# Optimization experiments

Hardware: AMD Instinct MI355X
Metric: run time of the kernel (lower is better)

Reference implementation:

```python
import jax, jax.numpy as jnp
import numpy as np

B, T, SEQ = 8, 129, 128
H, N, NL, NE, V = 512, 64, 4, 128, 18

def _gelu(x):
    return jax.nn.gelu(x, approximate=False)

def _conv2d(x, w, b, stride):
    y = jax.lax.conv_general_dilated(x, w, (stride, stride), 'VALID',
                                     dimension_numbers=('NCHW', 'OIHW', 'NCHW'))
    return y + b[None, :, None, None]

def _layernorm(x, g, b, eps=1e-5):
    mu = jnp.mean(x, axis=-1, keepdims=True)
    var = jnp.mean(jnp.square(x - mu), axis=-1, keepdims=True)
    return (x - mu) * jax.lax.rsqrt(var + eps) * g + b

def _s4_kernel(log_dt, A_re, A_im, C_re, C_im, L):
    # Diagonal SSM (ZOH discretization, B=1): K[h,l] = 2*Re(sum_n Ceff * exp(dt*A)^l)
    dt = jnp.exp(log_dt)[:, None]                  # [H,1]
    A = A_re + 1j * A_im                            # [H,N] complex64
    dtA = (dt * A).astype(jnp.complex64)
    C = (C_re + 1j * C_im).astype(jnp.complex64)
    Ceff = C * (jnp.exp(dtA) - 1.0) / A             # [H,N]
    vand = jnp.exp(dtA[:, :, None] * jnp.arange(L, dtype=jnp.float32))  # [H,N,L]
    return 2.0 * jnp.einsum('hn,hnl->hl', Ceff, vand).real

def _fft_conv(u, K, D):
    # u: [B,H,L]  K: [H,L]  causal conv via zero-padded FFT
    L = u.shape[-1]
    n = 2 * L
    Uf = jnp.fft.rfft(u, n=n)
    Kf = jnp.fft.rfft(K, n=n)
    y = jnp.fft.irfft(Uf * Kf[None], n=n)[..., :L]
    return y + D[None, :, None] * u

def setup_inputs() -> dict:
    key = jax.random.key(0)
    ks = jax.random.split(key, 32)
    d = {}
    d['states'] = jax.random.uniform(ks[0], (B, T, 4, 84, 84), dtype=jnp.float32)
    d['actions'] = jax.random.randint(ks[1], (B, T), 0, V)
    d['rtgs'] = jax.random.uniform(ks[2], (B, T, 1), dtype=jnp.float32)
    s = 0.02
    d['enc_w1'] = jax.random.normal(ks[3], (32, 4, 8, 8)) * s
    d['enc_b1'] = jnp.zeros((32,))
    d['enc_w2'] = jax.random.normal(ks[4], (64, 32, 4, 4)) * s
    d['enc_b2'] = jnp.zeros((64,))
    d['enc_w3'] = jax.random.normal(ks[5], (64, 64, 3, 3)) * s
    d['enc_b3'] = jnp.zeros((64,))
    d['enc_lw'] = jax.random.normal(ks[6], (3136, NE)) * s
    d['enc_lb'] = jnp.zeros((NE,))
    d['ret_w'] = jax.random.normal(ks[7], (1, NE)) * s
    d['ret_b'] = jnp.zeros((NE,))
    d['act_emb'] = jax.random.normal(ks[8], (V, NE)) * s
    d['proj_w'] = jax.random.normal(ks[9], (3 * NE, H)) * s
    d['proj_b'] = jnp.zeros((H,))
    d['pre_w'] = jax.random.normal(ks[10], (H, H)) * s
    d['pre_b'] = jnp.zeros((H,))
    d['ln_g'] = jnp.ones((NL, H))
    d['ln_b'] = jnp.zeros((NL, H))
    lo, hi = np.log(1e-3), np.log(1e-1)
    d['log_dt'] = lo + jax.random.uniform(ks[11], (NL, H)) * (hi - lo)
    d['A_re'] = -0.5 * jnp.ones((NL, H, N))
    d['A_im'] = jnp.broadcast_to(np.pi * jnp.arange(N, dtype=jnp.float32), (NL, H, N)).copy()
    d['C_re'] = jax.random.normal(ks[12], (NL, H, N)) * (0.5 ** 0.5)
    d['C_im'] = jax.random.normal(ks[13], (NL, H, N)) * (0.5 ** 0.5)
    d['Dp'] = jax.random.normal(ks[14], (NL, H))
    d['aft_w'] = jax.random.normal(ks[15], (NL, H, H)) * s
    d['aft_b'] = jnp.zeros((NL, H))
    d['out_w'] = jax.random.normal(ks[16], (H, V)) * s
    return d

def reference(states, actions, rtgs, enc_w1, enc_b1, enc_w2, enc_b2, enc_w3, enc_b3,
              enc_lw, enc_lb, ret_w, ret_b, act_emb, proj_w, proj_b, pre_w, pre_b,
              ln_g, ln_b, log_dt, A_re, A_im, C_re, C_im, Dp, aft_w, aft_b, out_w):
    S = actions.shape[1] - 1  # del_r = 1
    # state encoder over B*S frames
    x = states[:, 1:].reshape(-1, 4, 84, 84)
    x = jax.nn.relu(_conv2d(x, enc_w1, enc_b1, 4))
    x = jax.nn.relu(_conv2d(x, enc_w2, enc_b2, 2))
    x = jax.nn.relu(_conv2d(x, enc_w3, enc_b3, 1))
    se = jnp.tanh(x.reshape(x.shape[0], -1) @ enc_lw + enc_lb)          # [B*S, NE]
    ae = jnp.tanh(act_emb[actions[:, :S].reshape(-1)])                   # [B*S, NE]
    re = jnp.tanh(rtgs[:, :S].reshape(-1, 1) @ ret_w + ret_b)            # [B*S, NE]
    u = jnp.concatenate([se, ae, re], axis=-1) @ proj_w + proj_b
    u = u.reshape(states.shape[0], S, H)
    y = _gelu(u) @ pre_w + pre_b                                          # beforeblock
    for i in range(NL):
        r = _layernorm(y, ln_g[i], ln_b[i])
        v = jnp.transpose(r, (0, 2, 1))                                   # [B,H,S]
        K = _s4_kernel(log_dt[i], A_re[i], A_im[i], C_re[i], C_im[i], S)
        c = _fft_conv(v, K, Dp[i])
        c = jnp.transpose(c, (0, 2, 1))                                   # [B,S,H]
        c = _gelu(_gelu(c) @ aft_w[i] + aft_b[i])
        y = c + y                                                          # s4_resnet
    logits = y @ out_w                                                     # [B,S,V]
    return logits
```

## Files before the change

### kernel.cpp

```cpp
#include <hip/hip_runtime.h>

#define Bq 8
#define Tq 129
#define Sq 128
#define Hq 512
#define Nq 64
#define NLq 4
#define NEq 128
#define Vq 18

typedef unsigned short u16;
typedef unsigned int u32;
typedef __attribute__((ext_vector_type(8))) short short8v;
typedef __attribute__((ext_vector_type(4))) float f32x4;

__device__ __forceinline__ float gelu_f(float x) {
  return 0.5f * x * (1.0f + erff(x * 0.70710678118654752f));
}

__device__ __forceinline__ u16 f2b(float x) {
  union { float f; unsigned int u; } v; v.f = x;
  unsigned int r = v.u + 0x7FFFu + ((v.u >> 16) & 1u);
  return (u16)(r >> 16);
}

__device__ __forceinline__ float b2f_lo(u32 u) {
  union { unsigned int u; float f; } v; v.u = u << 16; return v.f;
}
__device__ __forceinline__ float b2f_hi(u32 u) {
  union { unsigned int u; float f; } v; v.u = u & 0xffff0000u; return v.f;
}

__global__ __launch_bounds__(256) void prep_k(
    const float* __restrict__ enc_lw, const float* __restrict__ proj_w,
    const float* __restrict__ pre_w, const float* __restrict__ aft_w,
    const float* __restrict__ out_w,
    const float* __restrict__ w1, const float* __restrict__ w2,
    const float* __restrict__ w3,
    u16* __restrict__ Wt_enc, u16* __restrict__ Wt_proj, u16* __restrict__ Wt_pre,
    u16* __restrict__ Wt_aft, u16* __restrict__ Wt_out,
    u16* __restrict__ B1t, u16* __restrict__ B2t, u16* __restrict__ B3t) {
  __shared__ u16 T[64][65];
  int bid = blockIdx.x;
  if (bid >= 474) {
    int i = (bid - 474) * 256 + threadIdx.x;
    if (i < 8192) {
      int n = i >> 8, k = i & 255;
      int ic = k >> 6, ky = (k >> 3) & 7, kx = k & 7;
      B1t[i] = f2b(w1[((n * 4 + ic) * 8 + ky) * 8 + kx]);
    } else if (i < 8192 + 32768) {
      int j = i - 8192;
      int n = j >> 9, k = j & 511;
      int kyx = k >> 5, ic = k & 31, ky = kyx >> 2, kx = kyx & 3;
      B2t[j] = f2b(w2[((n * 32 + ic) * 4 + ky) * 4 + kx]);
    } else if (i < 8192 + 32768 + 36864) {
      int j = i - 40960;
      int n = j / 576, k = j - n * 576;
      int ic = k & 63, kyx = k >> 6, ky = kyx / 3, kx = kyx % 3;
      B3t[j] = f2b(w3[((n * 64 + ic) * 3 + ky) * 3 + kx]);
    }
    return;
  }
  const float* src; u16* dst; int K, N, kt, nt, t;
  if (bid < 98)       { t = bid;       src = enc_lw; dst = Wt_enc;  K = 3136; N = 128; kt = t >> 1; nt = t & 1; }
  else if (bid < 146) { t = bid - 98;  src = proj_w; dst = Wt_proj; K = 384;  N = 512; kt = t >> 3; nt = t & 7; }
  else if (bid < 210) { t = bid - 146; src = pre_w;  dst = Wt_pre;  K = 512;  N = 512; kt = t >> 3; nt = t & 7; }
  else if (bid < 466) { t = bid - 210; int L = t >> 6; t &= 63;
                        src = aft_w + (size_t)L * 262144; dst = Wt_aft + (size_t)L * 262144;
                        K = 512; N = 512; kt = t >> 3; nt = t & 7; }
  else                { t = bid - 466; src = out_w;  dst = Wt_out;  K = 512;  N = 18;  kt = t;      nt = 0; }
  int k0 = kt * 64, n0 = nt * 64;
  #pragma unroll
  for (int it = 0; it < 16; it++) {
    int idx = it * 256 + threadIdx.x;
    int rr = idx >> 6, cc = idx & 63;
    float v = (n0 + cc < N) ? src[(size_t)(k0 + rr) * N + n0 + cc] : 0.f;
    T[cc][rr] = f2b(v);
  }
  __syncthreads();
  #pragma unroll
  for (int it = 0; it < 16; it++) {
    int idx = it * 256 + threadIdx.x;
    int rr = idx >> 6, cc = idx & 63;
    dst[(size_t)(n0 + rr) * K + k0 + cc] = T[rr][cc];
  }
}

template<bool AF32, int EPI>
__global__ __launch_bounds__(256) void mgemm(const void* __restrict__ Av,
    const u16* __restrict__ Wt, const float* __restrict__ bias,
    const float* __restrict__ res, void* __restrict__ Cv,
    int M, int K, int N, int ldc) {
  __shared__ u16 As[4][64][40];
  __shared__ u16 Bs[4][64][40];
  int tid = threadIdx.x;
  int bn = blockIdx.x * 64, bm = blockIdx.y * 64;
  int lane = tid & 63, w = tid >> 6;
  int q = lane >> 4, r = lane & 15;
  int wm = (w >> 1) * 32, wn = (w & 1) * 32;
  int am = tid >> 2, ak0 = (tid & 3) * 8;
  f32x4 acc[2][2] = {};
  for (int k0 = 0; k0 < K; k0 += 128) {
    #pragma unroll
    for (int st = 0; st < 4; st++) {
      int kk = k0 + st * 32 + ak0;
      if constexpr (AF32) {
        const float* A = (const float*)Av;
        const float* src = A + (size_t)(bm + am) * K + kk;
        float4 v0 = *(const float4*)src;
        float4 v1 = *(const float4*)(src + 4);
        ushort4 lo, hi;
        lo.x = f2b(v0.x); lo.y = f2b(v0.y); lo.z = f2b(v0.z); lo.w = f2b(v0.w);
        hi.x = f2b(v1.x); hi.y = f2b(v1.y); hi.z = f2b(v1.z); hi.w = f2b(v1.w);
        *(ushort4*)&As[st][am][ak0] = lo;
        *(ushort4*)&As[st][am][ak0 + 4] = hi;
      } else {
        *(short8v*)&As[st][am][ak0] =
            *(const short8v*)((const u16*)Av + (size_t)(bm + am) * K + kk);
      }
      *(short8v*)&Bs[st][am][ak0] = *(const short8v*)(Wt + (size_t)(bn + am) * K + kk);
    }
    __syncthreads();
    #pragma unroll
    for (int st = 0; st < 4; st++) {
      short8v a0 = *(const short8v*)&As[st][wm + r][q * 8];
      short8v a1 = *(const short8v*)&As[st][wm + 16 + r][q * 8];
      short8v b0 = *(const short8v*)&Bs[st][wn + r][q * 8];
      short8v b1 = *(const short8v*)&Bs[st][wn + 16 + r][q * 8];
      acc[0][0] = __builtin_amdgcn_mfma_f32_16x16x32_bf16(a0, b0, acc[0][0], 0, 0, 0);
      acc[0][1] = __builtin_amdgcn_mfma_f32_16x16x32_bf16(a0, b1, acc[0][1], 0, 0, 0);
      acc[1][0] = __builtin_amdgcn_mfma_f32_16x16x32_bf16(a1, b0, acc[1][0], 0, 0, 0);
      acc[1][1] = __builtin_amdgcn_mfma_f32_16x16x32_bf16(a1, b1, acc[1][1], 0, 0, 0);
    }
    __syncthreads();
  }
  #pragma unroll
  for (int ms = 0; ms < 2; ms++) {
    #pragma unroll
    for (int ns = 0; ns < 2; ns++) {
      #pragma unroll
      for (int reg = 0; reg < 4; reg++) {
        int m = bm + wm + ms * 16 + q * 4 + reg;
        int n = bn + wn + ns * 16 + r;
        if (n < N) {
          float v = acc[ms][ns][reg] + (bias ? bias[n] : 0.f);
          if (EPI == 0) ((float*)Cv)[(size_t)m * ldc + n] = v;
          if (EPI == 2) ((u16*)Cv)[(size_t)m * ldc + n] = f2b(gelu_f(v));
          if (EPI == 3) ((float*)Cv)[(size_t)m * ldc + n] = gelu_f(v) + res[(size_t)m * ldc + n];
        }
      }
    }
  }
}

__global__ __launch_bounds__(256) void enc_gemm(const u16* __restrict__ A,
    const u16* __restrict__ Wt, float* __restrict__ Cp) {
  __shared__ u16 As[64][40];
  __shared__ u16 Bs[64][40];
  int tid = threadIdx.x;
  int bn = blockIdx.x * 64, bm = blockIdx.y * 64, kc = blockIdx.z;
  int lane = tid & 63, w = tid >> 6;
  int q = lane >> 4, r = lane & 15;
  int wm = (w >> 1) * 32, wn = (w & 1) * 32;
  int am = tid >> 2, ak = (tid & 3) * 8;
  f32x4 acc[2][2] = {};
  int kend = kc * 448 + 448;
  for (int k0 = kc * 448; k0 < kend; k0 += 32) {
    *(short8v*)&As[am][ak] = *(const short8v*)(A + (size_t)(bm + am) * 3136 + k0 + ak);
    *(short8v*)&Bs[am][ak] = *(const short8v*)(Wt + (size_t)(bn + am) * 3136 + k0 + ak);
    __syncthreads();
    short8v a0 = *(const short8v*)&As[wm + r][q * 8];
    short8v a1 = *(const short8v*)&As[wm + 16 + r][q * 8];
    short8v b0 = *(const short8v*)&Bs[wn + r][q * 8];
    short8v b1 = *(const short8v*)&Bs[wn + 16 + r][q * 8];
    acc[0][0] = __builtin_amdgcn_mfma_f32_16x16x32_bf16(a0, b0, acc[0][0], 0, 0, 0);
    acc[0][1] = __builtin_amdgcn_mfma_f32_16x16x32_bf16(a0, b1, acc[0][1], 0, 0, 0);
    acc[1][0] = __builtin_amdgcn_mfma_f32_16x16x32_bf16(a1, b0, acc[1][0], 0, 0, 0);
    acc[1][1] = __builtin_amdgcn_mfma_f32_16x16x32_bf16(a1, b1, acc[1][1], 0, 0, 0);
    __syncthreads();
  }
  #pragma unroll
  for (int ms = 0; ms < 2; ms++)
    #pragma unroll
    for (int ns = 0; ns < 2; ns++)
      #pragma unroll
      for (int reg = 0; reg < 4; reg++) {
        int m = bm + wm + ms * 16 + q * 4 + reg;
        int n = bn + wn + ns * 16 + r;
        Cp[(size_t)(kc * 1024 + m) * 128 + n] = acc[ms][ns][reg];
      }
}

__global__ __launch_bounds__(256) void embedred_k(const float* __restrict__ Cp,
    const float* __restrict__ enc_lb, const int* __restrict__ actions,
    const float* __restrict__ rtgs, const float* __restrict__ act_emb,
    const float* __restrict__ ret_w, const float* __restrict__ ret_b,
    u16* __restrict__ uin) {
  int f = blockIdx.x;
  int b = f >> 7, s = f & 127;
  int e = threadIdx.x;
  if (e < 128) {
    float sum = enc_lb[e];
    #pragma unroll
    for (int kc = 0; kc < 7; kc++) sum += Cp[(size_t)(kc * 1024 + f) * 128 + e];
    uin[(size_t)f * 384 + e] = f2b(tanhf(sum));
    uin[(size_t)f * 384 + 256 + e] =
        f2b(tanhf(fmaf(rtgs[b * Tq + s], ret_w[e], ret_b[e])));
  } else {
    int ee = e - 128;
    int a = actions[b * Tq + s];
    uin[(size_t)f * 384 + 128 + ee] = f2b(tanhf(act_emb[a * NEq + ee]));
  }
}

__global__ __launch_bounds__(512) void conv1_mfma(const float* __restrict__ states,
    const u16* __restrict__ B1t, const float* __restrict__ bias, u16* __restrict__ out) {
  __shared__ u16 lds[28224];
  int fr = blockIdx.x;
  int b = fr >> 7, s = fr & 127;
  const float* in = states + (size_t)(b * Tq + s + 1) * 28224;
  int tid = threadIdx.x;
  #pragma unroll
  for (int it = 0; it < 14; it++) {
    int idx = tid + it * 512;
    if (idx < 7056) {
      float4 v = ((const float4*)in)[idx];
      ushort4 uv;
      uv.x = f2b(v.x); uv.y = f2b(v.y); uv.z = f2b(v.z); uv.w = f2b(v.w);
      *(ushort4*)&lds[idx * 4] = uv;
    }
  }
  int lane = tid & 63, w = tid >> 6;
  int q = lane >> 4, r = lane & 15;
  short8v bfr[2][8];
  #pragma unroll
  for (int nt = 0; nt < 2; nt++)
    #pragma unroll
    for (int ks = 0; ks < 8; ks++)
      bfr[nt][ks] = *(const short8v*)(B1t + (nt * 16 + r) * 256 + ks * 32 + q * 8);
  __syncthreads();
  for (int mt = w; mt < 25; mt += 8) {
    int m = mt * 16 + r;
    int oy = m / 20, ox = m % 20;
    f32x4 acc0 = {0.f, 0.f, 0.f, 0.f}, acc1 = {0.f, 0.f, 0.f, 0.f};
    #pragma unroll
    for (int ks = 0; ks < 8; ks++) {
      int k0 = ks * 32 + q * 8;
      int ic = k0 >> 6, ky = (k0 >> 3) & 7;
      int ai = ic * 7056 + (oy * 4 + ky) * 84 + ox * 4;
      ushort4 lo = *(const ushort4*)&lds[ai];
      ushort4 hi = *(const ushort4*)&lds[ai + 4];
      short8v av;
      av[0] = (short)lo.x; av[1] = (short)lo.y; av[2] = (short)lo.z; av[3] = (short)lo.w;
      av[4] = (short)hi.x; av[5] = (short)hi.y; av[6] = (short)hi.z; av[7] = (short)hi.w;
      acc0 = __builtin_amdgcn_mfma_f32_16x16x32_bf16(av, bfr[0][ks], acc0, 0, 0, 0);
      acc1 = __builtin_amdgcn_mfma_f32_16x16x32_bf16(av, bfr[1][ks], acc1, 0, 0, 0);
    }
    #pragma unroll
    for (int reg = 0; reg < 4; reg++) {
      int pos = mt * 16 + q * 4 + reg;
      out[(size_t)fr * 12800 + pos * 32 + r]      = f2b(fmaxf(acc0[reg] + bias[r], 0.f));
      out[(size_t)fr * 12800 + pos * 32 + 16 + r] = f2b(fmaxf(acc1[reg] + bias[16 + r], 0.f));
    }
  }
}

__global__ __launch_bounds__(256) void conv2_mfma(const u16* __restrict__ in_,
    const u16* __restrict__ B2t, const float* __restrict__ bias, u16* __restrict__ out) {
  __shared__ u16 lds[12800];
  int fr = blockIdx.x;
  int tid = threadIdx.x;
  const short8v* src = (const short8v*)(in_ + (size_t)fr * 12800);
  short8v* dst = (short8v*)lds;
  #pragma unroll
  for (int it = 0; it < 7; it++) {
    int idx = tid + it * 256;
    if (idx < 1600) dst[idx] = src[idx];
  }
  int lane = tid & 63, w = tid >> 6;
  int q = lane >> 4, r = lane & 15;
  int n = w * 16 + r;
  short8v bfr[16];
  #pragma unroll
  for (int ks = 0; ks < 16; ks++)
    bfr[ks] = *(const short8v*)(B2t + n * 512 + ks * 32 + q * 8);
  __syncthreads();
  float bn = bias[n];
  #pragma unroll
  for (int mt = 0; mt < 6; mt++) {
    int m = mt * 16 + r; if (m > 80) m = 80;
    int oy = m / 9, ox = m % 9;
    f32x4 acc = {0.f, 0.f, 0.f, 0.f};
    #pragma unroll
    for (int ks = 0; ks < 16; ks++) {
      int ky = ks >> 2, kx = ks & 3;
      int ai = ((oy * 2 + ky) * 20 + ox * 2 + kx) * 32 + q * 8;
      short8v av = *(const short8v*)&lds[ai];
      acc = __builtin_amdgcn_mfma_f32_16x16x32_bf16(av, bfr[ks], acc, 0, 0, 0);
    }
    #pragma unroll
    for (int reg = 0; reg < 4; reg++) {
      int pos = mt * 16 + q * 4 + reg;
      if (pos < 81)
        out[(size_t)fr * 5184 + pos * 64 + n] = f2b(fmaxf(acc[reg] + bn, 0.f));
    }
  }
}

__global__ __launch_bounds__(256) void conv3_mfma(const u16* __restrict__ in_,
    const u16* __restrict__ B3t, const float* __restrict__ bias, u16* __restrict__ out) {
  __shared__ u16 lds[5184];
  int fr = blockIdx.x;
  int tid = threadIdx.x;
  const short8v* src = (const short8v*)(in_ + (size_t)fr * 5184);
  short8v* dst = (short8v*)lds;
  #pragma unroll
  for (int it = 0; it < 3; it++) {
    int idx = tid + it * 256;
    if (idx < 648) dst[idx] = src[idx];
  }
  int lane = tid & 63, w = tid >> 6;
  int q = lane >> 4, r = lane & 15;
  int n = w * 16 + r;
  short8v bfr[18];
  #pragma unroll
  for (int ks = 0; ks < 18; ks++)
    bfr[ks] = *(const short8v*)(B3t + n * 576 + ks * 32 + q * 8);
  __syncthreads();
  float bn = bias[n];
  #pragma unroll
  for (int mt = 0; mt < 4; mt++) {
    int m = mt * 16 + r; if (m > 48) m = 48;
    int oy = m / 7, ox = m % 7;
    f32x4 acc = {0.f, 0.f, 0.f, 0.f};
    #pragma unroll
    for (int ks = 0; ks < 18; ks++) {
      int kyx = ks >> 1;
      int ky = kyx / 3, kx = kyx % 3;
      int ic0 = (ks & 1) * 32 + q * 8;
      int ai = ((oy + ky) * 9 + ox + kx) * 64 + ic0;
      short8v av = *(const short8v*)&lds[ai];
      acc = __builtin_amdgcn_mfma_f32_16x16x32_bf16(av, bfr[ks], acc, 0, 0, 0);
    }
    #pragma unroll
    for (int reg = 0; reg < 4; reg++) {
      int pos = mt * 16 + q * 4 + reg;
      if (pos < 49)
        out[(size_t)fr * 3136 + n * 49 + pos] = f2b(fmaxf(acc[reg] + bn, 0.f));
    }
  }
}

__global__ __launch_bounds__(64) void s4k_gen(const float* __restrict__ log_dt,
    const float* __restrict__ A_re, const float* __restrict__ A_im,
    const float* __restrict__ C_re, const float* __restrict__ C_im,
    u16* __restrict__ Ktb) {
  __shared__ float con[64][129];
  int lh = blockIdx.x;
  int n = threadIdx.x;
  float dt = expf(log_dt[lh]);
  float ar = A_re[(size_t)lh * Nq + n], ai = A_im[(size_t)lh * Nq + n];
  float al = dt * ar, be = dt * ai;
  float er = expf(al);
  float wr = er * cosf(be), wi = er * sinf(be);
  float zr = wr - 1.0f, zi = wi;
  float den = 1.0f / (ar * ar + ai * ai);
  float tr = (zr * ar + zi * ai) * den, ti = (zi * ar - zr * ai) * den;
  float Cr = C_re[(size_t)lh * Nq + n], Ci = C_im[(size_t)lh * Nq + n];
  float cr = Cr * tr - Ci * ti, ci = Cr * ti + Ci * tr;
  float curr = 1.0f, curi = 0.0f;
  for (int l = 0; l < Sq; l++) {
    con[n][l] = cr * curr - ci * curi;
    float nr = curr * wr - curi * wi;
    curi = curr * wi + curi * wr;
    curr = nr;
  }
  __syncthreads();
  int layer = lh >> 9, h = lh & 511;
  #pragma unroll
  for (int li = n; li < Sq; li += 64) {
    float s = 0.f;
    for (int j = 0; j < 64; j++) s += con[j][li];
    Ktb[((size_t)layer * Sq + li) * Hq + h] = f2b(2.0f * s);
  }
}

__global__ __launch_bounds__(256) void ln_stats(const float* __restrict__ y,
    float2* __restrict__ stats) {
  int row = blockIdx.x * 4 + (threadIdx.x >> 6);
  int lane = threadIdx.x & 63;
  const float* x = y + (size_t)row * Hq;
  float s = 0.f, s2 = 0.f;
  #pragma unroll
  for (int j = 0; j < 8; j++) {
    float v = x[lane + j * 64];
    s += v; s2 += v * v;
  }
  #pragma unroll
  for (int o = 32; o >= 1; o >>= 1) {
    s += __shfl_xor(s, o);
    s2 += __shfl_xor(s2, o);
  }
  if (lane == 0) {
    float mu = s * (1.f / Hq);
    float var = s2 * (1.f / Hq) - mu * mu;
    stats[row] = make_float2(mu, rsqrtf(var + 1e-5f));
  }
}

__global__ __launch_bounds__(256) void sconv_fused(const float* __restrict__ y,
    const float2* __restrict__ stats, const float* __restrict__ g,
    const float* __restrict__ bta, const u16* __restrict__ Kt,
    const float* __restrict__ D, u16* __restrict__ cact) {
  __shared__ u32 P[16][140];
  __shared__ u32 KL[16][132];
  int hc = blockIdx.x, b = blockIdx.y;
  int t = threadIdx.x;
  int h0 = hc * 32;
  if (t < 16) {
    #pragma unroll
    for (int i = 0; i < 8; i++) P[t][i] = 0;
  }
  #pragma unroll
  for (int it = 0; it < 8; it++) {
    int idx = it * 256 + t;
    int p = idx & 15, j = idx >> 4;
    KL[p][j] = *(const u32*)(Kt + (size_t)j * Hq + h0 + 2 * p);
  }
  #pragma unroll
  for (int it = 0; it < 8; it++) {
    int idx = it * 256 + t;
    int p = idx & 15, s = idx >> 4;
    int row = b * Sq + s;
    float2 v = *(const float2*)(y + (size_t)row * Hq + h0 + 2 * p);
    float2 st = stats[row];
    float2 gg = *(const float2*)(g + h0 + 2 * p);
    float2 bb = *(const float2*)(bta + h0 + 2 * p);
    float r0 = (v.x - st.x) * st.y * gg.x + bb.x;
    float r1 = (v.y - st.x) * st.y * gg.y + bb.y;
    P[p][8 + s] = (u32)f2b(r0) | ((u32)f2b(r1) << 16);
  }
  __syncthreads();
  int p = t & 15, sg = t >> 4;
  int s0 = sg * 8;
  float acc0[8], acc1[8];
  float2 d2 = *(const float2*)(D + h0 + 2 * p);
  #pragma unroll
  for (int k = 0; k < 8; k++) {
    u32 rv = P[p][8 + s0 + k];
    acc0[k] = d2.x * b2f_lo(rv);
    acc1[k] = d2.y * b2f_hi(rv);
  }
  for (int jb = 0; jb <= sg; jb++) {
    int base = (sg - jb) * 8;
    u32 wv[16], kv[8];
    *(uint4*)&wv[0]  = *(const uint4*)&P[p][base];
    *(uint4*)&wv[4]  = *(const uint4*)&P[p][base + 4];
    *(uint4*)&wv[8]  = *(const uint4*)&P[p][base + 8];
    *(uint4*)&wv[12] = *(const uint4*)&P[p][base + 12];
    *(uint4*)&kv[0]  = *(const uint4*)&KL[p][jb * 8];
    *(uint4*)&kv[4]  = *(const uint4*)&KL[p][jb * 8 + 4];
    float wlo[16], whi[16], klo[8], khi[8];
    #pragma unroll
    for (int i = 0; i < 16; i++) { wlo[i] = b2f_lo(wv[i]); whi[i] = b2f_hi(wv[i]); }
    #pragma unroll
    for (int i = 0; i < 8; i++) { klo[i] = b2f_lo(kv[i]); khi[i] = b2f_hi(kv[i]); }
    #pragma unroll
    for (int jo = 0; jo < 8; jo++)
      #pragma unroll
      for (int k = 0; k < 8; k++) {
        acc0[k] = fmaf(klo[jo], wlo[8 + k - jo], acc0[k]);
        acc1[k] = fmaf(khi[jo], whi[8 + k - jo], acc1[k]);
      }
  }
  #pragma unroll
  for (int k = 0; k < 8; k++) {
    int s = s0 + k;
    u32 outv = (u32)f2b(gelu_f(acc0[k])) | ((u32)f2b(gelu_f(acc1[k])) << 16);
    *(u32*)(cact + ((size_t)(b * Sq + s)) * Hq + h0 + 2 * p) = outv;
  }
}

extern "C" void kernel_launch(void* const* d_in, const int* in_sizes, int n_in,
                              void* d_out, int out_size, void* d_ws, size_t ws_size,
                              hipStream_t stream) {
  const float* states  = (const float*)d_in[0];
  const int*   actions = (const int*)  d_in[1];
  const float* rtgs    = (const float*)d_in[2];
  const float* enc_w1  = (const float*)d_in[3];
  const float* enc_b1  = (const float*)d_in[4];
  const float* enc_w2  = (const float*)d_in[5];
  const float* enc_b2  = (const float*)d_in[6];
  const float* enc_w3  = (const float*)d_in[7];
  const float* enc_b3  = (const float*)d_in[8];
  const float* enc_lw  = (const float*)d_in[9];
  const float* enc_lb  = (const float*)d_in[10];
  const float* ret_w   = (const float*)d_in[11];
  const float* ret_b   = (const float*)d_in[12];
  const float* act_emb = (const float*)d_in[13];
  const float* proj_w  = (const float*)d_in[14];
  const float* proj_b  = (const float*)d_in[15];
  const float* pre_w   = (const float*)d_in[16];
  const float* pre_b   = (const float*)d_in[17];
  const float* ln_g    = (const float*)d_in[18];
  const float* ln_b    = (const float*)d_in[19];
  const float* log_dt  = (const float*)d_in[20];
  const float* A_re    = (const float*)d_in[21];
  const float* A_im    = (const float*)d_in[22];
  const float* C_re    = (const float*)d_in[23];
  const float* C_im    = (const float*)d_in[24];
  const float* Dp      = (const float*)d_in[25];
  const float* aft_w   = (const float*)d_in[26];
  const float* aft_b   = (const float*)d_in[27];
  const float* out_w   = (const float*)d_in[28];

  u16* Wt_enc  = (u16*)d_ws;
  u16* Wt_proj = Wt_enc + 401408;
  u16* Wt_pre  = Wt_proj + 196608;
  u16* Wt_aft  = Wt_pre + 262144;
  u16* Wt_out  = Wt_aft + 1048576;
  u16* B1t = Wt_out + 32768;
  u16* B2t = B1t + 8192;
  u16* B3t = B2t + 32768;
  u16* o1  = B3t + 36864;
  u16* o2  = o1 + 13107200;
  u16* x3b = o2 + 5308416;
  u16* uin = x3b + 3211264;
  u16* uact = uin + 393216;
  u16* cact = uact + 524288;
  u16* Ktb  = cact + 524288;
  float* y    = (float*)(Ktb + 262144);
  float* Cp   = y + 524288;
  float2* stats = (float2*)(Cp + 917504);

  prep_k<<<778, 256, 0, stream>>>(enc_lw, proj_w, pre_w, aft_w, out_w,
                                  enc_w1, enc_w2, enc_w3,
                                  Wt_enc, Wt_proj, Wt_pre, Wt_aft, Wt_out,
                                  B1t, B2t, B3t);
  conv1_mfma<<<1024, 512, 0, stream>>>(states, B1t, enc_b1, o1);
  conv2_mfma<<<1024, 256, 0, stream>>>(o1, B2t, enc_b2, o2);
  conv3_mfma<<<1024, 256, 0, stream>>>(o2, B3t, enc_b3, x3b);
  enc_gemm<<<dim3(2, 16, 7), 256, 0, stream>>>(x3b, Wt_enc, Cp);
  embedred_k<<<1024, 256, 0, stream>>>(Cp, enc_lb, actions, rtgs, act_emb,
                                       ret_w, ret_b, uin);
  mgemm<false, 2><<<dim3(8, 16), 256, 0, stream>>>(uin, Wt_proj, proj_b, nullptr, uact,
                                                   1024, 384, 512, 512);
  mgemm<false, 0><<<dim3(8, 16), 256, 0, stream>>>(uact, Wt_pre, pre_b, nullptr, y,
                                                   1024, 512, 512, 512);
  s4k_gen<<<2048, 64, 0, stream>>>(log_dt, A_re, A_im, C_re, C_im, Ktb);

  for (int i = 0; i < NLq; i++) {
    ln_stats<<<256, 256, 0, stream>>>(y, stats);
    sconv_fused<<<dim3(16, 8), 256, 0, stream>>>(y, stats, ln_g + i * Hq,
                                                 ln_b + i * Hq,
                                                 Ktb + (size_t)i * Sq * Hq,
                                                 Dp + i * Hq, cact);
    mgemm<false, 3><<<dim3(8, 16), 256, 0, stream>>>(cact, Wt_aft + (size_t)i * Hq * Hq,
                                                     aft_b + i * Hq, y, y,
                                                     1024, 512, 512, 512);
  }
  mgemm<true, 0><<<dim3(1, 16), 256, 0, stream>>>(y, Wt_out, nullptr, nullptr,
                                                  (float*)d_out, 1024, 512, Vq, Vq);
}
```

Measured before the change: 225.8 us.

## Fuse the three conv layers into one kernel and fold layernorm stats into the GEMM epilogue

Merges conv1, conv2 and conv3 into a single per-frame kernel that keeps the intermediate activations in LDS, so the o1 and o2 tensors no longer round-trip through global memory. The separate ln_stats kernel is also removed. Instead, the GEMM epilogues that produce y write per-row partial sums and sums of squares, and sconv_fused reduces those partials into mean and rstd. This cuts memory traffic and several launches. In exchange the fused conv kernel uses much more LDS, which may lower occupancy, and the later conv stages run with a different wave partitioning.

```diff
diff --git a/kernel.cpp b/kernel.cpp
--- a/kernel.cpp
+++ b/kernel.cpp
@@ -86,11 +86,11 @@
   }
 }
 
-template<bool AF32, int EPI>
+template<bool AF32, int EPI, bool STATS>
 __global__ __launch_bounds__(256) void mgemm(const void* __restrict__ Av,
     const u16* __restrict__ Wt, const float* __restrict__ bias,
     const float* __restrict__ res, void* __restrict__ Cv,
-    int M, int K, int N, int ldc) {
+    float2* __restrict__ part, int M, int K, int N, int ldc) {
   __shared__ u16 As[4][64][40];
   __shared__ u16 Bs[4][64][40];
   int tid = threadIdx.x;
@@ -134,6 +134,7 @@
     }
     __syncthreads();
   }
+  float yv[2][2][4];
   #pragma unroll
   for (int ms = 0; ms < 2; ms++) {
     #pragma unroll
@@ -144,9 +145,31 @@
         int n = bn + wn + ns * 16 + r;
         if (n < N) {
           float v = acc[ms][ns][reg] + (bias ? bias[n] : 0.f);
-          if (EPI == 0) ((float*)Cv)[(size_t)m * ldc + n] = v;
+          if (EPI == 0) { ((float*)Cv)[(size_t)m * ldc + n] = v; yv[ms][ns][reg] = v; }
           if (EPI == 2) ((u16*)Cv)[(size_t)m * ldc + n] = f2b(gelu_f(v));
-          if (EPI == 3) ((float*)Cv)[(size_t)m * ldc + n] = gelu_f(v) + res[(size_t)m * ldc + n];
+          if (EPI == 3) {
+            float o = gelu_f(v) + res[(size_t)m * ldc + n];
+            ((float*)Cv)[(size_t)m * ldc + n] = o; yv[ms][ns][reg] = o;
+          }
+        }
+      }
+    }
+  }
+  if constexpr (STATS) {
+    #pragma unroll
+    for (int ms = 0; ms < 2; ms++) {
+      #pragma unroll
+      for (int reg = 0; reg < 4; reg++) {
+        float s = yv[ms][0][reg] + yv[ms][1][reg];
+        float s2 = yv[ms][0][reg] * yv[ms][0][reg] + yv[ms][1][reg] * yv[ms][1][reg];
+        #pragma unroll
+        for (int o = 1; o <= 8; o <<= 1) {
+          s += __shfl_xor(s, o);
+          s2 += __shfl_xor(s2, o);
+        }
+        if (r == 0) {
+          int m = bm + wm + ms * 16 + q * 4 + reg;
+          part[(size_t)(blockIdx.x * 2 + (w & 1)) * 1024 + m] = make_float2(s, s2);
         }
       }
     }
@@ -213,9 +236,12 @@
   }
 }
 
-__global__ __launch_bounds__(512) void conv1_mfma(const float* __restrict__ states,
-    const u16* __restrict__ B1t, const float* __restrict__ bias, u16* __restrict__ out) {
-  __shared__ u16 lds[28224];
+__global__ __launch_bounds__(512) void convs_mfma(const float* __restrict__ states,
+    const u16* __restrict__ B1t, const u16* __restrict__ B2t, const u16* __restrict__ B3t,
+    const float* __restrict__ b1, const float* __restrict__ b2, const float* __restrict__ b3,
+    u16* __restrict__ x3b) {
+  __shared__ u16 in_lds[28224];
+  __shared__ u16 o1_lds[12800];
   int fr = blockIdx.x;
   int b = fr >> 7, s = fr & 127;
   const float* in = states + (size_t)(b * Tq + s + 1) * 28224;
@@ -227,17 +253,17 @@
       float4 v = ((const float4*)in)[idx];
       ushort4 uv;
       uv.x = f2b(v.x); uv.y = f2b(v.y); uv.z = f2b(v.z); uv.w = f2b(v.w);
-      *(ushort4*)&lds[idx * 4] = uv;
+      *(ushort4*)&in_lds[idx * 4] = uv;
     }
   }
   int lane = tid & 63, w = tid >> 6;
   int q = lane >> 4, r = lane & 15;
-  short8v bfr[2][8];
+  short8v bfr1[2][8];
   #pragma unroll
   for (int nt = 0; nt < 2; nt++)
     #pragma unroll
     for (int ks = 0; ks < 8; ks++)
-      bfr[nt][ks] = *(const short8v*)(B1t + (nt * 16 + r) * 256 + ks * 32 + q * 8);
+      bfr1[nt][ks] = *(const short8v*)(B1t + (nt * 16 + r) * 256 + ks * 32 + q * 8);
   __syncthreads();
   for (int mt = w; mt < 25; mt += 8) {
     int m = mt * 16 + r;
@@ -248,46 +274,32 @@
       int k0 = ks * 32 + q * 8;
       int ic = k0 >> 6, ky = (k0 >> 3) & 7;
       int ai = ic * 7056 + (oy * 4 + ky) * 84 + ox * 4;
-      ushort4 lo = *(const ushort4*)&lds[ai];
-      ushort4 hi = *(const ushort4*)&lds[ai + 4];
+      ushort4 lo = *(const ushort4*)&in_lds[ai];
+      ushort4 hi = *(const ushort4*)&in_lds[ai + 4];
       short8v av;
       av[0] = (short)lo.x; av[1] = (short)lo.y; av[2] = (short)lo.z; av[3] = (short)lo.w;
       av[4] = (short)hi.x; av[5] = (short)hi.y; av[6] = (short)hi.z; av[7] = (short)hi.w;
-      acc0 = __builtin_amdgcn_mfma_f32_16x16x32_bf16(av, bfr[0][ks], acc0, 0, 0, 0);
-      acc1 = __builtin_amdgcn_mfma_f32_16x16x32_bf16(av, bfr[1][ks], acc1, 0, 0, 0);
+      acc0 = __builtin_amdgcn_mfma_f32_16x16x32_bf16(av, bfr1[0][ks], acc0, 0, 0, 0);
+      acc1 = __builtin_amdgcn_mfma_f32_16x16x32_bf16(av, bfr1[1][ks], acc1, 0, 0, 0);
     }
     #pragma unroll
     for (int reg = 0; reg < 4; reg++) {
       int pos = mt * 16 + q * 4 + reg;
-      out[(size_t)fr * 12800 + pos * 32 + r]      = f2b(fmaxf(acc0[reg] + bias[r], 0.f));
-      out[(size_t)fr * 12800 + pos * 32 + 16 + r] = f2b(fmaxf(acc1[reg] + bias[16 + r], 0.f));
-    }
-  }
-}
-
-__global__ __launch_bounds__(256) void conv2_mfma(const u16* __restrict__ in_,
-    const u16* __restrict__ B2t, const float* __restrict__ bias, u16* __restrict__ out) {
-  __shared__ u16 lds[12800];
-  int fr = blockIdx.x;
-  int tid = threadIdx.x;
-  const short8v* src = (const short8v*)(in_ + (size_t)fr * 12800);
-  short8v* dst = (short8v*)lds;
-  #pragma unroll
-  for (int it = 0; it < 7; it++) {
-    int idx = tid + it * 256;
-    if (idx < 1600) dst[idx] = src[idx];
-  }
-  int lane = tid & 63, w = tid >> 6;
-  int q = lane >> 4, r = lane & 15;
-  int n = w * 16 + r;
-  short8v bfr[16];
+      o1_lds[pos * 32 + r]      = f2b(fmaxf(acc0[reg] + b1[r], 0.f));
+      o1_lds[pos * 32 + 16 + r] = f2b(fmaxf(acc1[reg] + b1[16 + r], 0.f));
+    }
+  }
+  int nt2 = w & 3, g2 = w >> 2;
+  int n2 = nt2 * 16 + r;
+  short8v bfr2[16];
   #pragma unroll
   for (int ks = 0; ks < 16; ks++)
-    bfr[ks] = *(const short8v*)(B2t + n * 512 + ks * 32 + q * 8);
-  __syncthreads();
-  float bn = bias[n];
-  #pragma unroll
-  for (int mt = 0; mt < 6; mt++) {
+    bfr2[ks] = *(const short8v*)(B2t + n2 * 512 + ks * 32 + q * 8);
+  __syncthreads();
+  float bn2 = b2[n2];
+  #pragma unroll
+  for (int j = 0; j < 3; j++) {
+    int mt = g2 * 3 + j;
     int m = mt * 16 + r; if (m > 80) m = 80;
     int oy = m / 9, ox = m % 9;
     f32x4 acc = {0.f, 0.f, 0.f, 0.f};
@@ -295,41 +307,26 @@
     for (int ks = 0; ks < 16; ks++) {
       int ky = ks >> 2, kx = ks & 3;
       int ai = ((oy * 2 + ky) * 20 + ox * 2 + kx) * 32 + q * 8;
-      short8v av = *(const short8v*)&lds[ai];
-      acc = __builtin_amdgcn_mfma_f32_16x16x32_bf16(av, bfr[ks], acc, 0, 0, 0);
+      short8v av = *(const short8v*)&o1_lds[ai];
+      acc = __builtin_amdgcn_mfma_f32_16x16x32_bf16(av, bfr2[ks], acc, 0, 0, 0);
     }
     #pragma unroll
     for (int reg = 0; reg < 4; reg++) {
       int pos = mt * 16 + q * 4 + reg;
       if (pos < 81)
-        out[(size_t)fr * 5184 + pos * 64 + n] = f2b(fmaxf(acc[reg] + bn, 0.f));
-    }
-  }
-}
-
-__global__ __launch_bounds__(256) void conv3_mfma(const u16* __restrict__ in_,
-    const u16* __restrict__ B3t, const float* __restrict__ bias, u16* __restrict__ out) {
-  __shared__ u16 lds[5184];
-  int fr = blockIdx.x;
-  int tid = threadIdx.x;
-  const short8v* src = (const short8v*)(in_ + (size_t)fr * 5184);
-  short8v* dst = (short8v*)lds;
-  #pragma unroll
-  for (int it = 0; it < 3; it++) {
-    int idx = tid + it * 256;
-    if (idx < 648) dst[idx] = src[idx];
-  }
-  int lane = tid & 63, w = tid >> 6;
-  int q = lane >> 4, r = lane & 15;
-  int n = w * 16 + r;
-  short8v bfr[18];
+        in_lds[pos * 64 + n2] = f2b(fmaxf(acc[reg] + bn2, 0.f));
+    }
+  }
+  short8v bfr3[18];
   #pragma unroll
   for (int ks = 0; ks < 18; ks++)
-    bfr[ks] = *(const short8v*)(B3t + n * 576 + ks * 32 + q * 8);
-  __syncthreads();
-  float bn = bias[n];
-  #pragma unroll
-  for (int mt = 0; mt < 4; mt++) {
+    bfr3[ks] = *(const short8v*)(B3t + n2 * 576 + ks * 32 + q * 8);
+  __syncthreads();
+  float bn3 = b3[n2];
+  int g3 = w >> 2;
+  #pragma unroll
+  for (int j = 0; j < 2; j++) {
+    int mt = g3 * 2 + j;
     int m = mt * 16 + r; if (m > 48) m = 48;
     int oy = m / 7, ox = m % 7;
     f32x4 acc = {0.f, 0.f, 0.f, 0.f};
@@ -339,14 +336,14 @@
       int ky = kyx / 3, kx = kyx % 3;
       int ic0 = (ks & 1) * 32 + q * 8;
       int ai = ((oy + ky) * 9 + ox + kx) * 64 + ic0;
-      short8v av = *(const short8v*)&lds[ai];
-      acc = __builtin_amdgcn_mfma_f32_16x16x32_bf16(av, bfr[ks], acc, 0, 0, 0);
+      short8v av = *(const short8v*)&in_lds[ai];
+      acc = __builtin_amdgcn_mfma_f32_16x16x32_bf16(av, bfr3[ks], acc, 0, 0, 0);
     }
     #pragma unroll
     for (int reg = 0; reg < 4; reg++) {
       int pos = mt * 16 + q * 4 + reg;
       if (pos < 49)
-        out[(size_t)fr * 3136 + n * 49 + pos] = f2b(fmaxf(acc[reg] + bn, 0.f));
+        x3b[(size_t)fr * 3136 + n2 * 49 + pos] = f2b(fmaxf(acc[reg] + bn3, 0.f));
     }
   }
 }
@@ -385,38 +382,27 @@
   }
 }
 
-__global__ __launch_bounds__(256) void ln_stats(const float* __restrict__ y,
-    float2* __restrict__ stats) {
-  int row = blockIdx.x * 4 + (threadIdx.x >> 6);
-  int lane = threadIdx.x & 63;
-  const float* x = y + (size_t)row * Hq;
-  float s = 0.f, s2 = 0.f;
-  #pragma unroll
-  for (int j = 0; j < 8; j++) {
-    float v = x[lane + j * 64];
-    s += v; s2 += v * v;
-  }
-  #pragma unroll
-  for (int o = 32; o >= 1; o >>= 1) {
-    s += __shfl_xor(s, o);
-    s2 += __shfl_xor(s2, o);
-  }
-  if (lane == 0) {
-    float mu = s * (1.f / Hq);
-    float var = s2 * (1.f / Hq) - mu * mu;
-    stats[row] = make_float2(mu, rsqrtf(var + 1e-5f));
-  }
-}
-
 __global__ __launch_bounds__(256) void sconv_fused(const float* __restrict__ y,
-    const float2* __restrict__ stats, const float* __restrict__ g,
+    const float2* __restrict__ part, const float* __restrict__ g,
     const float* __restrict__ bta, const u16* __restrict__ Kt,
     const float* __restrict__ D, u16* __restrict__ cact) {
   __shared__ u32 P[16][140];
   __shared__ u32 KL[16][132];
+  __shared__ float2 statl[128];
   int hc = blockIdx.x, b = blockIdx.y;
   int t = threadIdx.x;
   int h0 = hc * 32;
+  if (t < 128) {
+    float s = 0.f, s2 = 0.f;
+    #pragma unroll
+    for (int pc = 0; pc < 16; pc++) {
+      float2 pp = part[(size_t)pc * 1024 + b * Sq + t];
+      s += pp.x; s2 += pp.y;
+    }
+    float mu = s * (1.f / Hq);
+    float var = s2 * (1.f / Hq) - mu * mu;
+    statl[t] = make_float2(mu, rsqrtf(var + 1e-5f));
+  }
   if (t < 16) {
     #pragma unroll
     for (int i = 0; i < 8; i++) P[t][i] = 0;
@@ -427,13 +413,14 @@
     int p = idx & 15, j = idx >> 4;
     KL[p][j] = *(const u32*)(Kt + (size_t)j * Hq + h0 + 2 * p);
   }
+  __syncthreads();
   #pragma unroll
   for (int it = 0; it < 8; it++) {
     int idx = it * 256 + t;
     int p = idx & 15, s = idx >> 4;
     int row = b * Sq + s;
     float2 v = *(const float2*)(y + (size_t)row * Hq + h0 + 2 * p);
-    float2 st = stats[row];
+    float2 st = statl[s];
     float2 gg = *(const float2*)(g + h0 + 2 * p);
     float2 bb = *(const float2*)(bta + h0 + 2 * p);
     float r0 = (v.x - st.x) * st.y * gg.x + bb.x;
@@ -522,43 +509,39 @@
   u16* B1t = Wt_out + 32768;
   u16* B2t = B1t + 8192;
   u16* B3t = B2t + 32768;
-  u16* o1  = B3t + 36864;
-  u16* o2  = o1 + 13107200;
-  u16* x3b = o2 + 5308416;
+  u16* x3b = B3t + 36864;
   u16* uin = x3b + 3211264;
   u16* uact = uin + 393216;
   u16* cact = uact + 524288;
   u16* Ktb  = cact + 524288;
   float* y    = (float*)(Ktb + 262144);
   float* Cp   = y + 524288;
-  float2* stats = (float2*)(Cp + 917504);
+  float2* part = (float2*)(Cp + 917504);
 
   prep_k<<<778, 256, 0, stream>>>(enc_lw, proj_w, pre_w, aft_w, out_w,
                                   enc_w1, enc_w2, enc_w3,
                                   Wt_enc, Wt_proj, Wt_pre, Wt_aft, Wt_out,
                                   B1t, B2t, B3t);
-  conv1_mfma<<<1024, 512, 0, stream>>>(states, B1t, enc_b1, o1);
-  conv2_mfma<<<1024, 256, 0, stream>>>(o1, B2t, enc_b2, o2);
-  conv3_mfma<<<1024, 256, 0, stream>>>(o2, B3t, enc_b3, x3b);
+  convs_mfma<<<1024, 512, 0, stream>>>(states, B1t, B2t, B3t,
+                                       enc_b1, enc_b2, enc_b3, x3b);
   enc_gemm<<<dim3(2, 16, 7), 256, 0, stream>>>(x3b, Wt_enc, Cp);
   embedred_k<<<1024, 256, 0, stream>>>(Cp, enc_lb, actions, rtgs, act_emb,
                                        ret_w, ret_b, uin);
-  mgemm<false, 2><<<dim3(8, 16), 256, 0, stream>>>(uin, Wt_proj, proj_b, nullptr, uact,
-                                                   1024, 384, 512, 512);
-  mgemm<false, 0><<<dim3(8, 16), 256, 0, stream>>>(uact, Wt_pre, pre_b, nullptr, y,
-                                                   1024, 512, 512, 512);
+  mgemm<false, 2, false><<<dim3(8, 16), 256, 0, stream>>>(uin, Wt_proj, proj_b,
+      nullptr, uact, nullptr, 1024, 384, 512, 512);
+  mgemm<false, 0, true><<<dim3(8, 16), 256, 0, stream>>>(uact, Wt_pre, pre_b,
+      nullptr, y, part, 1024, 512, 512, 512);
   s4k_gen<<<2048, 64, 0, stream>>>(log_dt, A_re, A_im, C_re, C_im, Ktb);
 
   for (int i = 0; i < NLq; i++) {
-    ln_stats<<<256, 256, 0, stream>>>(y, stats);
-    sconv_fused<<<dim3(16, 8), 256, 0, stream>>>(y, stats, ln_g + i * Hq,
+    sconv_fused<<<dim3(16, 8), 256, 0, stream>>>(y, part, ln_g + i * Hq,
                                                  ln_b + i * Hq,
                                                  Ktb + (size_t)i * Sq * Hq,
                                                  Dp + i * Hq, cact);
-    mgemm<false, 3><<<dim3(8, 16), 256, 0, stream>>>(cact, Wt_aft + (size_t)i * Hq * Hq,
-                                                     aft_b + i * Hq, y, y,
-                                                     1024, 512, 512, 512);
-  }
-  mgemm<true, 0><<<dim3(1, 16), 256, 0, stream>>>(y, Wt_out, nullptr, nullptr,
-                                                  (float*)d_out, 1024, 512, Vq, Vq);
-}
+    mgemm<false, 3, true><<<dim3(8, 16), 256, 0, stream>>>(cact,
+        Wt_aft + (size_t)i * Hq * Hq, aft_b + i * Hq, y, y, part,
+        1024, 512, 512, 512);
+  }
+  mgemm<true, 0, false><<<dim3(1, 16), 256, 0, stream>>>(y, Wt_out, nullptr,
+      nullptr, (float*)d_out, nullptr, 1024, 512, Vq, Vq);
+}
```

New measurement: 240.0 us. +6.3%, slower.

## Fuse layernorm statistics into GEMM epilogue and split conv1 across two blocks

Applied to the files above, without the earlier changes.

Removes the separate ln_stats kernel. The pre and aft GEMM epilogues now write per-row partial sums and sums of squares, and sconv_fused reduces the 16 partials per row into mean and rstd in shared memory. Separately, conv1 is split into two half-frame blocks of 256 threads with a smaller LDS footprint, which aims to raise occupancy and parallelism. The cost is some duplicated input loading for the overlapping rows of the two halves, plus small extra epilogue work and register use in the GEMM.

```diff
diff --git a/kernel.cpp b/kernel.cpp
--- a/kernel.cpp
+++ b/kernel.cpp
@@ -86,11 +86,11 @@
   }
 }
 
-template<bool AF32, int EPI>
+template<bool AF32, int EPI, bool STATS>
 __global__ __launch_bounds__(256) void mgemm(const void* __restrict__ Av,
     const u16* __restrict__ Wt, const float* __restrict__ bias,
     const float* __restrict__ res, void* __restrict__ Cv,
-    int M, int K, int N, int ldc) {
+    float2* __restrict__ part, int M, int K, int N, int ldc) {
   __shared__ u16 As[4][64][40];
   __shared__ u16 Bs[4][64][40];
   int tid = threadIdx.x;
@@ -134,6 +134,7 @@
     }
     __syncthreads();
   }
+  float yv[2][2][4];
   #pragma unroll
   for (int ms = 0; ms < 2; ms++) {
     #pragma unroll
@@ -144,9 +145,31 @@
         int n = bn + wn + ns * 16 + r;
         if (n < N) {
           float v = acc[ms][ns][reg] + (bias ? bias[n] : 0.f);
-          if (EPI == 0) ((float*)Cv)[(size_t)m * ldc + n] = v;
+          if (EPI == 0) { ((float*)Cv)[(size_t)m * ldc + n] = v; yv[ms][ns][reg] = v; }
           if (EPI == 2) ((u16*)Cv)[(size_t)m * ldc + n] = f2b(gelu_f(v));
-          if (EPI == 3) ((float*)Cv)[(size_t)m * ldc + n] = gelu_f(v) + res[(size_t)m * ldc + n];
+          if (EPI == 3) {
+            float o = gelu_f(v) + res[(size_t)m * ldc + n];
+            ((float*)Cv)[(size_t)m * ldc + n] = o; yv[ms][ns][reg] = o;
+          }
+        }
+      }
+    }
+  }
+  if constexpr (STATS) {
+    #pragma unroll
+    for (int ms = 0; ms < 2; ms++) {
+      #pragma unroll
+      for (int reg = 0; reg < 4; reg++) {
+        float s = yv[ms][0][reg] + yv[ms][1][reg];
+        float s2 = yv[ms][0][reg] * yv[ms][0][reg] + yv[ms][1][reg] * yv[ms][1][reg];
+        #pragma unroll
+        for (int o = 1; o <= 8; o <<= 1) {
+          s += __shfl_xor(s, o);
+          s2 += __shfl_xor(s2, o);
+        }
+        if (r == 0) {
+          int m = bm + wm + ms * 16 + q * 4 + reg;
+          part[(size_t)(blockIdx.x * 2 + (w & 1)) * 1024 + m] = make_float2(s, s2);
         }
       }
     }
@@ -213,21 +236,24 @@
   }
 }
 
-__global__ __launch_bounds__(512) void conv1_mfma(const float* __restrict__ states,
+__global__ __launch_bounds__(256) void conv1_mfma(const float* __restrict__ states,
     const u16* __restrict__ B1t, const float* __restrict__ bias, u16* __restrict__ out) {
-  __shared__ u16 lds[28224];
-  int fr = blockIdx.x;
+  __shared__ u16 lds[4][3696];
+  int blk = blockIdx.x;
+  int fr = blk >> 1, half = blk & 1;
   int b = fr >> 7, s = fr & 127;
-  const float* in = states + (size_t)(b * Tq + s + 1) * 28224;
+  const float* in = states + (size_t)(b * Tq + s + 1) * 28224 + half * 3360;
   int tid = threadIdx.x;
   #pragma unroll
-  for (int it = 0; it < 14; it++) {
-    int idx = tid + it * 512;
-    if (idx < 7056) {
-      float4 v = ((const float4*)in)[idx];
+  for (int it = 0; it < 15; it++) {
+    int idx = tid + it * 256;
+    if (idx < 3696) {
+      int ic = idx >> 2; ic = idx / 924;
+      int r2 = idx - ic * 924;
+      float4 v = *(const float4*)(in + ic * 7056 + r2 * 4);
       ushort4 uv;
       uv.x = f2b(v.x); uv.y = f2b(v.y); uv.z = f2b(v.z); uv.w = f2b(v.w);
-      *(ushort4*)&lds[idx * 4] = uv;
+      *(ushort4*)&lds[ic][r2 * 4] = uv;
     }
   }
   int lane = tid & 63, w = tid >> 6;
@@ -239,17 +265,17 @@
     for (int ks = 0; ks < 8; ks++)
       bfr[nt][ks] = *(const short8v*)(B1t + (nt * 16 + r) * 256 + ks * 32 + q * 8);
   __syncthreads();
-  for (int mt = w; mt < 25; mt += 8) {
-    int m = mt * 16 + r;
-    int oy = m / 20, ox = m % 20;
+  for (int mt = w; mt < 13; mt += 4) {
+    int m = mt * 16 + r; if (m > 199) m = 199;
+    int oyl = m / 20, ox = m % 20;
     f32x4 acc0 = {0.f, 0.f, 0.f, 0.f}, acc1 = {0.f, 0.f, 0.f, 0.f};
     #pragma unroll
     for (int ks = 0; ks < 8; ks++) {
       int k0 = ks * 32 + q * 8;
       int ic = k0 >> 6, ky = (k0 >> 3) & 7;
-      int ai = ic * 7056 + (oy * 4 + ky) * 84 + ox * 4;
-      ushort4 lo = *(const ushort4*)&lds[ai];
-      ushort4 hi = *(const ushort4*)&lds[ai + 4];
+      int ai = (oyl * 4 + ky) * 84 + ox * 4;
+      ushort4 lo = *(const ushort4*)&lds[ic][ai];
+      ushort4 hi = *(const ushort4*)&lds[ic][ai + 4];
       short8v av;
       av[0] = (short)lo.x; av[1] = (short)lo.y; av[2] = (short)lo.z; av[3] = (short)lo.w;
       av[4] = (short)hi.x; av[5] = (short)hi.y; av[6] = (short)hi.z; av[7] = (short)hi.w;
@@ -259,8 +285,11 @@
     #pragma unroll
     for (int reg = 0; reg < 4; reg++) {
       int pos = mt * 16 + q * 4 + reg;
-      out[(size_t)fr * 12800 + pos * 32 + r]      = f2b(fmaxf(acc0[reg] + bias[r], 0.f));
-      out[(size_t)fr * 12800 + pos * 32 + 16 + r] = f2b(fmaxf(acc1[reg] + bias[16 + r], 0.f));
+      if (pos < 200) {
+        int gp = half * 200 + pos;
+        out[(size_t)fr * 12800 + gp * 32 + r]      = f2b(fmaxf(acc0[reg] + bias[r], 0.f));
+        out[(size_t)fr * 12800 + gp * 32 + 16 + r] = f2b(fmaxf(acc1[reg] + bias[16 + r], 0.f));
+      }
     }
   }
 }
@@ -385,38 +414,27 @@
   }
 }
 
-__global__ __launch_bounds__(256) void ln_stats(const float* __restrict__ y,
-    float2* __restrict__ stats) {
-  int row = blockIdx.x * 4 + (threadIdx.x >> 6);
-  int lane = threadIdx.x & 63;
-  const float* x = y + (size_t)row * Hq;
-  float s = 0.f, s2 = 0.f;
-  #pragma unroll
-  for (int j = 0; j < 8; j++) {
-    float v = x[lane + j * 64];
-    s += v; s2 += v * v;
-  }
-  #pragma unroll
-  for (int o = 32; o >= 1; o >>= 1) {
-    s += __shfl_xor(s, o);
-    s2 += __shfl_xor(s2, o);
-  }
-  if (lane == 0) {
-    float mu = s * (1.f / Hq);
-    float var = s2 * (1.f / Hq) - mu * mu;
-    stats[row] = make_float2(mu, rsqrtf(var + 1e-5f));
-  }
-}
-
 __global__ __launch_bounds__(256) void sconv_fused(const float* __restrict__ y,
-    const float2* __restrict__ stats, const float* __restrict__ g,
+    const float2* __restrict__ part, const float* __restrict__ g,
     const float* __restrict__ bta, const u16* __restrict__ Kt,
     const float* __restrict__ D, u16* __restrict__ cact) {
   __shared__ u32 P[16][140];
   __shared__ u32 KL[16][132];
+  __shared__ float2 statl[128];
   int hc = blockIdx.x, b = blockIdx.y;
   int t = threadIdx.x;
   int h0 = hc * 32;
+  if (t < 128) {
+    float s = 0.f, s2 = 0.f;
+    #pragma unroll
+    for (int pc = 0; pc < 16; pc++) {
+      float2 pp = part[(size_t)pc * 1024 + b * Sq + t];
+      s += pp.x; s2 += pp.y;
+    }
+    float mu = s * (1.f / Hq);
+    float var = s2 * (1.f / Hq) - mu * mu;
+    statl[t] = make_float2(mu, rsqrtf(var + 1e-5f));
+  }
   if (t < 16) {
     #pragma unroll
     for (int i = 0; i < 8; i++) P[t][i] = 0;
@@ -427,13 +445,14 @@
     int p = idx & 15, j = idx >> 4;
     KL[p][j] = *(const u32*)(Kt + (size_t)j * Hq + h0 + 2 * p);
   }
+  __syncthreads();
   #pragma unroll
   for (int it = 0; it < 8; it++) {
     int idx = it * 256 + t;
     int p = idx & 15, s = idx >> 4;
     int row = b * Sq + s;
     float2 v = *(const float2*)(y + (size_t)row * Hq + h0 + 2 * p);
-    float2 st = stats[row];
+    float2 st = statl[s];
     float2 gg = *(const float2*)(g + h0 + 2 * p);
     float2 bb = *(const float2*)(bta + h0 + 2 * p);
     float r0 = (v.x - st.x) * st.y * gg.x + bb.x;
@@ -531,34 +550,33 @@
   u16* Ktb  = cact + 524288;
   float* y    = (float*)(Ktb + 262144);
   float* Cp   = y + 524288;
-  float2* stats = (float2*)(Cp + 917504);
+  float2* part = (float2*)(Cp + 917504);
 
   prep_k<<<778, 256, 0, stream>>>(enc_lw, proj_w, pre_w, aft_w, out_w,
                                   enc_w1, enc_w2, enc_w3,
                                   Wt_enc, Wt_proj, Wt_pre, Wt_aft, Wt_out,
                                   B1t, B2t, B3t);
-  conv1_mfma<<<1024, 512, 0, stream>>>(states, B1t, enc_b1, o1);
+  conv1_mfma<<<2048, 256, 0, stream>>>(states, B1t, enc_b1, o1);
   conv2_mfma<<<1024, 256, 0, stream>>>(o1, B2t, enc_b2, o2);
   conv3_mfma<<<1024, 256, 0, stream>>>(o2, B3t, enc_b3, x3b);
   enc_gemm<<<dim3(2, 16, 7), 256, 0, stream>>>(x3b, Wt_enc, Cp);
   embedred_k<<<1024, 256, 0, stream>>>(Cp, enc_lb, actions, rtgs, act_emb,
                                        ret_w, ret_b, uin);
-  mgemm<false, 2><<<dim3(8, 16), 256, 0, stream>>>(uin, Wt_proj, proj_b, nullptr, uact,
-                                                   1024, 384, 512, 512);
-  mgemm<false, 0><<<dim3(8, 16), 256, 0, stream>>>(uact, Wt_pre, pre_b, nullptr, y,
-                                                   1024, 512, 512, 512);
+  mgemm<false, 2, false><<<dim3(8, 16), 256, 0, stream>>>(uin, Wt_proj, proj_b,
+      nullptr, uact, nullptr, 1024, 384, 512, 512);
+  mgemm<false, 0, true><<<dim3(8, 16), 256, 0, stream>>>(uact, Wt_pre, pre_b,
+      nullptr, y, part, 1024, 512, 512, 512);
   s4k_gen<<<2048, 64, 0, stream>>>(log_dt, A_re, A_im, C_re, C_im, Ktb);
 
   for (int i = 0; i < NLq; i++) {
-    ln_stats<<<256, 256, 0, stream>>>(y, stats);
-    sconv_fused<<<dim3(16, 8), 256, 0, stream>>>(y, stats, ln_g + i * Hq,
+    sconv_fused<<<dim3(16, 8), 256, 0, stream>>>(y, part, ln_g + i * Hq,
                                                  ln_b + i * Hq,
                                                  Ktb + (size_t)i * Sq * Hq,
                                                  Dp + i * Hq, cact);
-    mgemm<false, 3><<<dim3(8, 16), 256, 0, stream>>>(cact, Wt_aft + (size_t)i * Hq * Hq,
-                                                     aft_b + i * Hq, y, y,
-                                                     1024, 512, 512, 512);
-  }
-  mgemm<true, 0><<<dim3(1, 16), 256, 0, stream>>>(y, Wt_out, nullptr, nullptr,
-                                                  (float*)d_out, 1024, 512, Vq, Vq);
-}
+    mgemm<false, 3, true><<<dim3(8, 16), 256, 0, stream>>>(cact,
+        Wt_aft + (size_t)i * Hq * Hq, aft_b + i * Hq, y, y, part,
+        1024, 512, 512, 512);
+  }
+  mgemm<true, 0, false><<<dim3(1, 16), 256, 0, stream>>>(y, Wt_out, nullptr,
+      nullptr, (float*)d_out, nullptr, 1024, 512, Vq, Vq);
+}
```

Result: slower. 235.8 us (+4.4%).
